# Optimization experiments

Measured on AMD Instinct MI355X. Metric: run time of the kernel, lower is better.

## Reference

```python
import jax, jax.numpy as jnp
import numpy as np

B, T, D, H = 2048, 512, 1, 36


def _lstm_dir(x, Wih, Whh, bih, bhh, reverse):
    # x: [B,T,Din]; Wih: [4H,Din]; Whh: [4H,H]. PyTorch gate order: i,f,g,o.
    # Precompute input projection for all timesteps (hoisted out of the scan).
    xp = jnp.einsum('btd,gd->btg', x, Wih) + (bih + bhh)  # [B,T,4H]
    xp = jnp.swapaxes(xp, 0, 1)  # [T,B,4H]
    if reverse:
        xp = xp[::-1]
    h0 = jnp.zeros((x.shape[0], Whh.shape[1]), x.dtype)

    def step(carry, xt):
        h, c = carry
        z = xt + h @ Whh.T  # [B,4H]
        i, f, g, o = jnp.split(z, 4, axis=-1)
        c = jax.nn.sigmoid(f) * c + jax.nn.sigmoid(i) * jnp.tanh(g)
        h = jax.nn.sigmoid(o) * jnp.tanh(c)
        return (h, c), h

    _, hs = jax.lax.scan(step, (h0, h0), xp)  # hs: [T,B,H]
    if reverse:
        hs = hs[::-1]
    return jnp.swapaxes(hs, 0, 1)  # [B,T,H]


def _bilstm_layer(x, pf, pr):
    hf = _lstm_dir(x, *pf, reverse=False)
    hr = _lstm_dir(x, *pr, reverse=True)
    return jnp.concatenate([hf, hr], axis=-1)  # [B,T,2H]


def setup_inputs() -> dict:
    key = jax.random.key(0)
    ks = jax.random.split(key, 20)
    bound = 1.0 / np.sqrt(H)  # PyTorch LSTM/Linear uniform init bound

    def u(k, shape):
        return jax.random.uniform(k, shape, jnp.float32, -bound, bound)

    inp = {"x": jax.random.normal(ks[0], (B, T, D), jnp.float32)}
    # layer 0 (input size D), forward and reverse directions
    inp["Wih0f"] = u(ks[1], (4 * H, D)); inp["Whh0f"] = u(ks[2], (4 * H, H))
    inp["bih0f"] = u(ks[3], (4 * H,));  inp["bhh0f"] = u(ks[4], (4 * H,))
    inp["Wih0r"] = u(ks[5], (4 * H, D)); inp["Whh0r"] = u(ks[6], (4 * H, H))
    inp["bih0r"] = u(ks[7], (4 * H,));  inp["bhh0r"] = u(ks[8], (4 * H,))
    # layer 1 (input size 2H)
    inp["Wih1f"] = u(ks[9], (4 * H, 2 * H)); inp["Whh1f"] = u(ks[10], (4 * H, H))
    inp["bih1f"] = u(ks[11], (4 * H,));      inp["bhh1f"] = u(ks[12], (4 * H,))
    inp["Wih1r"] = u(ks[13], (4 * H, 2 * H)); inp["Whh1r"] = u(ks[14], (4 * H, H))
    inp["bih1r"] = u(ks[15], (4 * H,));       inp["bhh1r"] = u(ks[16], (4 * H,))
    # fc head: Linear(2H -> 1)
    inp["fcW"] = u(ks[17], (1, 2 * H))
    inp["fcb"] = u(ks[18], (1,))
    return inp


def reference(x, Wih0f, Whh0f, bih0f, bhh0f, Wih0r, Whh0r, bih0r, bhh0r,
              Wih1f, Whh1f, bih1f, bhh1f, Wih1r, Whh1r, bih1r, bhh1r,
              fcW, fcb):
    out = _bilstm_layer(x, (Wih0f, Whh0f, bih0f, bhh0f),
                        (Wih0r, Whh0r, bih0r, bhh0r))
    out = _bilstm_layer(out, (Wih1f, Whh1f, bih1f, bhh1f),
                        (Wih1r, Whh1r, bih1r, bhh1r))
    return out[:, -1, :] @ fcW.T + fcb  # [B,1]
```

## Files before the change

kernel.cpp:

```cpp
#include <hip/hip_runtime.h>
#include <cstdint>

#define Hn 36
#define G4 144
#define TT 512
#define BB 2048

__device__ __forceinline__ float sigf(float x) { return 1.0f / (1.0f + __expf(-x)); }
__device__ __forceinline__ float tanh_fast(float x) {
    float e = __expf(2.0f * x);
    return 1.0f - 2.0f / (e + 1.0f);
}

#define REP9(M, P)  M(P,0) M(P,1) M(P,2) M(P,3) M(P,4) M(P,5) M(P,6) M(P,7) M(P,8)
#define DECLQ(P, i) float P##i##x, P##i##y, P##i##z, P##i##w;
#define LOADQ(P, i) { float4 _t = wp[i]; P##i##x = _t.x; P##i##y = _t.y; P##i##z = _t.z; P##i##w = _t.w; }
#define PINQ(P, i)  asm volatile("" : "+v"(P##i##x), "+v"(P##i##y), "+v"(P##i##z), "+v"(P##i##w));
#define FMAQ(P, i)                                                        \
    {  float4 hv = *(const float4*)&hb[(i) * 4];                          \
       z0 = fmaf(P##i##x, hv.x, z0); z1 = fmaf(P##i##y, hv.y, z1);        \
       z2 = fmaf(P##i##z, hv.z, z2); z3 = fmaf(P##i##w, hv.w, z3); }

#define DOT4Q(P, i)                                                       \
    {   float4 hA = *(const float4*)&hbb[0 * 40 + (i) * 4];               \
        A0 = fmaf(P##i##x, hA.x, A0); A1 = fmaf(P##i##y, hA.y, A1);       \
        A2 = fmaf(P##i##z, hA.z, A2); A3 = fmaf(P##i##w, hA.w, A3);       \
        float4 hB = *(const float4*)&hbb[1 * 40 + (i) * 4];               \
        B0 = fmaf(P##i##x, hB.x, B0); B1 = fmaf(P##i##y, hB.y, B1);       \
        B2 = fmaf(P##i##z, hB.z, B2); B3 = fmaf(P##i##w, hB.w, B3);       \
        float4 hC = *(const float4*)&hbb[2 * 40 + (i) * 4];               \
        C0 = fmaf(P##i##x, hC.x, C0); C1 = fmaf(P##i##y, hC.y, C1);       \
        C2 = fmaf(P##i##z, hC.z, C2); C3 = fmaf(P##i##w, hC.w, C3);       \
        float4 hD = *(const float4*)&hbb[3 * 40 + (i) * 4];               \
        D0 = fmaf(P##i##x, hD.x, D0); D1 = fmaf(P##i##y, hD.y, D1);       \
        D2 = fmaf(P##i##z, hD.z, D2); D3 = fmaf(P##i##w, hD.w, D3); }

#define DOT36(W, H, Z0, Z1, Z2, Z3)                        \
    do {                                                   \
        _Pragma("unroll") for (int _k = 0; _k < 9; ++_k) { \
            float4 hv = *(const float4*)&(H)[_k * 4];      \
            Z0 = fmaf((W)[_k * 4 + 0], hv.x, Z0);          \
            Z1 = fmaf((W)[_k * 4 + 1], hv.y, Z1);          \
            Z2 = fmaf((W)[_k * 4 + 2], hv.z, Z2);          \
            Z3 = fmaf((W)[_k * 4 + 3], hv.w, Z3);          \
        }                                                  \
    } while (0)

#define DOT72(W, H, Z0, Z1, Z2, Z3)                         \
    do {                                                    \
        _Pragma("unroll") for (int _k = 0; _k < 18; ++_k) { \
            float4 hv = *(const float4*)&(H)[_k * 4];       \
            Z0 = fmaf((W)[_k * 4 + 0], hv.x, Z0);           \
            Z1 = fmaf((W)[_k * 4 + 1], hv.y, Z1);           \
            Z2 = fmaf((W)[_k * 4 + 2], hv.z, Z2);           \
            Z3 = fmaf((W)[_k * 4 + 3], hv.w, Z3);           \
        }                                                   \
    } while (0)

#define SG1 4
#define NTK1 (SG1 * G4)
__global__ __launch_bounds__(NTK1) void l0rev_kernel(
    const float* __restrict__ x,
    const float* __restrict__ Wih, const float* __restrict__ Whh,
    const float* __restrict__ bih, const float* __restrict__ bhh,
    float* __restrict__ h0r)
{
    const int tid = threadIdx.x;
    const int cc  = tid / G4;
    const int g   = tid % G4;
    const int b   = blockIdx.x * SG1 + cc;

    __shared__ float xs[SG1][TT];
    __shared__ float hs[SG1][40];
    __shared__ float zs[SG1][G4];

    for (int i = g; i < TT; i += G4) xs[cc][i] = x[(size_t)b * TT + i];

    REP9(DECLQ, R)
    {
        const float4* wp = (const float4*)(Whh + g * Hn);
        REP9(LOADQ, R)
    }
    float wx   = Wih[g];
    float bias = bih[g] + bhh[g];
    REP9(PINQ, R)
    asm volatile("" : "+v"(wx), "+v"(bias));

    if (g < 40) hs[cc][g] = 0.0f;
    float c = 0.0f;
    __syncthreads();

    float* dst = h0r + (size_t)b * TT * Hn;

    for (int s = 0; s < TT; ++s) {
        const int t = TT - 1 - s;
        float z0 = fmaf(xs[cc][t], wx, bias), z1 = 0.f, z2 = 0.f, z3 = 0.f;
        {
            const float* hb = hs[cc];
            REP9(FMAQ, R)
        }
        zs[cc][g] = (z0 + z1) + (z2 + z3);
        __syncthreads();
        if (g < Hn) {
            float zi = zs[cc][g], zf = zs[cc][g + 36], zg = zs[cc][g + 72], zo = zs[cc][g + 108];
            c = sigf(zf) * c + sigf(zi) * tanh_fast(zg);
            float h = sigf(zo) * tanh_fast(c);
            hs[cc][g] = h;
            dst[(size_t)t * Hn + g] = h;
        }
        __syncthreads();
    }
}

#define SG2 4
#define NT2 576
__global__ __launch_bounds__(NT2) void fused_fl_kernel(
    const float* __restrict__ x,
    const float* __restrict__ Wih0f, const float* __restrict__ Whh0f,
    const float* __restrict__ bih0f, const float* __restrict__ bhh0f,
    const float* __restrict__ Wih1f, const float* __restrict__ Whh1f,
    const float* __restrict__ bih1f, const float* __restrict__ bhh1f,
    const float* __restrict__ Wih1r,
    const float* __restrict__ bih1r, const float* __restrict__ bhh1r,
    const float* __restrict__ fcW, const float* __restrict__ fcb,
    const float* __restrict__ h0r,
    float* __restrict__ out)
{
    const int tid  = threadIdx.x;
    const int gp   = tid / G4;
    const int g    = tid % G4;
    const int cc2  = g / Hn;
    const int ii   = g % Hn;
    const int base = blockIdx.x * SG2;

    __shared__ float xs[SG2][TT + 2];
    __shared__ float h0f[2][SG2][40];
    __shared__ float h0rs[2][SG2][40];
    __shared__ float h1s[SG2][40];
    __shared__ float zF[SG2][G4];
    __shared__ float zL[3][SG2][G4];
    __shared__ float red[SG2][40];

    for (int i = tid; i < SG2 * (TT + 2); i += NT2) {
        int c = i / (TT + 2), t = i % (TT + 2);
        xs[c][t] = (t < TT) ? x[(size_t)(base + c) * TT + t] : 0.0f;
    }
    for (int i = tid; i < 2 * SG2 * 40; i += NT2) {
        (&h0f[0][0][0])[i] = 0.0f;
        (&h0rs[0][0][0])[i] = 0.0f;
    }
    for (int i = tid; i < SG2 * 40; i += NT2) (&h1s[0][0])[i] = 0.0f;

    const float* wbase = (gp == 0) ? (Whh0f + g * Hn)
                       : (gp == 1) ? (Wih1f + g * 72)
                       : (gp == 2) ? (Wih1f + g * 72 + 36)
                                   : (Whh1f + g * Hn);
    REP9(DECLQ, W)
    {
        const float4* wp = (const float4*)wbase;
        REP9(LOADQ, W)
    }
    float wx0  = (gp == 0) ? Wih0f[g] : 0.0f;
    float bsum = (gp == 0) ? (bih0f[g] + bhh0f[g])
               : (gp == 3) ? (bih1f[g] + bhh1f[g]) : 0.0f;
    REP9(PINQ, W)
    asm volatile("" : "+v"(wx0), "+v"(bsum));

    const float* srow = h0r + (size_t)(base + cc2) * TT * Hn + ii;
    float c0 = 0.0f, c1 = 0.0f;
    __syncthreads();

    float rv = 0.0f;
    if (gp == 0) {
#pragma unroll
        for (int c = 0; c < SG2; ++c) zF[c][g] = fmaf(xs[c][0], wx0, bsum);
    } else if (gp == 2) {
        h0rs[0][cc2][ii] = srow[0];
        rv = srow[Hn];
    }
    __syncthreads();
    if (gp == 0) {
        float zi = zF[cc2][ii], zg = zF[cc2][ii + 72], zo = zF[cc2][ii + 108];
        c0 = sigf(zi) * tanh_fast(zg);
        h0f[0][cc2][ii] = sigf(zo) * tanh_fast(c0);
    }
    __syncthreads();

    int cur = 0;
    for (int t = 0; t < TT; ++t) {
        float rv2 = (gp == 2 && t + 2 < TT) ? srow[(size_t)(t + 2) * Hn] : 0.0f;

        const float* hbb = (gp <= 1) ? &h0f[cur][0][0]
                         : (gp == 2) ? &h0rs[cur][0][0] : &h1s[0][0];
        float A0, B0, C0, D0;
        if (gp == 0) {
            A0 = fmaf(xs[0][t + 1], wx0, bsum);
            B0 = fmaf(xs[1][t + 1], wx0, bsum);
            C0 = fmaf(xs[2][t + 1], wx0, bsum);
            D0 = fmaf(xs[3][t + 1], wx0, bsum);
        } else {
            A0 = bsum; B0 = bsum; C0 = bsum; D0 = bsum;
        }
        float A1 = 0.f, A2 = 0.f, A3 = 0.f, B1 = 0.f, B2 = 0.f, B3 = 0.f;
        float C1 = 0.f, C2 = 0.f, C3 = 0.f, D1 = 0.f, D2 = 0.f, D3 = 0.f;

        REP9(DOT4Q, W)

        float zA = (A0 + A1) + (A2 + A3);
        float zB = (B0 + B1) + (B2 + B3);
        float zC = (C0 + C1) + (C2 + C3);
        float zD = (D0 + D1) + (D2 + D3);
        if (gp == 0) {
            zF[0][g] = zA; zF[1][g] = zB; zF[2][g] = zC; zF[3][g] = zD;
        } else {
            float* zt = &zL[gp - 1][0][0];
            zt[0 * G4 + g] = zA; zt[1 * G4 + g] = zB;
            zt[2 * G4 + g] = zC; zt[3 * G4 + g] = zD;
        }
        __syncthreads();

        if (gp == 0) {
            if (t + 1 < TT) {
                float zi = zF[cc2][ii],       zf = zF[cc2][ii + 36];
                float zg = zF[cc2][ii + 72],  zo = zF[cc2][ii + 108];
                c0 = sigf(zf) * c0 + sigf(zi) * tanh_fast(zg);
                h0f[cur ^ 1][cc2][ii] = sigf(zo) * tanh_fast(c0);
            }
        } else if (gp == 3) {
            float zi = zL[0][cc2][ii]       + zL[1][cc2][ii]       + zL[2][cc2][ii];
            float zf = zL[0][cc2][ii + 36]  + zL[1][cc2][ii + 36]  + zL[2][cc2][ii + 36];
            float zg = zL[0][cc2][ii + 72]  + zL[1][cc2][ii + 72]  + zL[2][cc2][ii + 72];
            float zo = zL[0][cc2][ii + 108] + zL[1][cc2][ii + 108] + zL[2][cc2][ii + 108];
            c1 = sigf(zf) * c1 + sigf(zi) * tanh_fast(zg);
            h1s[cc2][ii] = sigf(zo) * tanh_fast(c1);
        } else if (gp == 2 && t + 1 < TT) {
            h0rs[cur ^ 1][cc2][ii] = rv;
        }
        __syncthreads();
        rv = rv2;
        if (t + 1 < TT) cur ^= 1;
    }

    {
        float zR = bih1r[g] + bhh1r[g];
        const float* wr = Wih1r + g * 72;
#pragma unroll
        for (int k = 0; k < Hn; ++k) zR = fmaf(wr[k],      h0f[cur][gp][k],  zR);
#pragma unroll
        for (int k = 0; k < Hn; ++k) zR = fmaf(wr[36 + k], h0rs[cur][gp][k], zR);
        zF[gp][g] = zR;
    }
    __syncthreads();
    if (tid < SG2 * Hn) {
        int c = tid / Hn, i = tid % Hn;
        float zi = zF[c][i], zg = zF[c][i + 72], zo = zF[c][i + 108];
        float cR = sigf(zi) * tanh_fast(zg);
        float hR = sigf(zo) * tanh_fast(cR);
        red[c][i] = fcW[36 + i] * hR + fcW[i] * h1s[c][i];
    }
    __syncthreads();
    if (tid < SG2) {
        float s2 = fcb[0];
        for (int j = 0; j < Hn; ++j) s2 += red[tid][j];
        out[base + tid] = s2;
    }
}

__global__ __launch_bounds__(G4, 1) void fused_all_kernel(
    const float* __restrict__ x,
    const float* __restrict__ Wih0f, const float* __restrict__ Whh0f,
    const float* __restrict__ bih0f, const float* __restrict__ bhh0f,
    const float* __restrict__ Wih0r, const float* __restrict__ Whh0r,
    const float* __restrict__ bih0r, const float* __restrict__ bhh0r,
    const float* __restrict__ Wih1f, const float* __restrict__ Whh1f,
    const float* __restrict__ bih1f, const float* __restrict__ bhh1f,
    const float* __restrict__ Wih1r,
    const float* __restrict__ bih1r, const float* __restrict__ bhh1r,
    const float* __restrict__ fcW, const float* __restrict__ fcb,
    float* __restrict__ out)
{
    const int g = threadIdx.x;
    const int b = blockIdx.x;

    __shared__ float xs[TT];
    __shared__ float cbuf[64][Hn];
    __shared__ float ckpt_h[8][Hn], ckpt_c[8][Hn];
    __shared__ float hr[40], h0s[80], hs1[40], zs[G4], red[40];

    for (int i = g; i < TT; i += G4) xs[i] = x[(size_t)b * TT + i];

    float wr[Hn], wf[Hn];
#pragma unroll
    for (int k = 0; k < Hn; ++k) wr[k] = Whh0r[g * Hn + k];
#pragma unroll
    for (int k = 0; k < Hn; ++k) wf[k] = Whh0f[g * Hn + k];
    const float wxr = Wih0r[g], br = bih0r[g] + bhh0r[g];
    const float wxf = Wih0f[g], bf = bih0f[g] + bhh0f[g];
    float w1i[72];
#pragma unroll
    for (int k = 0; k < 72; ++k) w1i[k] = Wih1f[g * 72 + k];
    float w1h[Hn];
#pragma unroll
    for (int k = 0; k < Hn; ++k) w1h[k] = Whh1f[g * Hn + k];
    const float b1 = bih1f[g] + bhh1f[g];

    if (g < Hn) hr[g] = 0.0f;
    float cr = 0.0f;
    __syncthreads();
    for (int s = 0; s < TT; ++s) {
        const int t = TT - 1 - s;
        if ((t & 63) == 63 && g < Hn) { ckpt_h[t >> 6][g] = hr[g]; ckpt_c[t >> 6][g] = cr; }
        float z0 = fmaf(xs[t], wxr, br), z1 = 0.f, z2 = 0.f, z3 = 0.f;
        DOT36(wr, hr, z0, z1, z2, z3);
        zs[g] = (z0 + z1) + (z2 + z3);
        __syncthreads();
        if (g < Hn) {
            float zi = zs[g], zf = zs[g + 36], zg = zs[g + 72], zo = zs[g + 108];
            cr = sigf(zf) * cr + sigf(zi) * tanh_fast(zg);
            hr[g] = sigf(zo) * tanh_fast(cr);
        }
        __syncthreads();
    }

    if (g < Hn) { h0s[g] = 0.0f; hs1[g] = 0.0f; }
    float c0 = 0.0f, c1 = 0.0f;
    __syncthreads();

    for (int m = 0; m < 8; ++m) {
        if (g < Hn) { hr[g] = ckpt_h[m][g]; cr = ckpt_c[m][g]; }
        __syncthreads();
        for (int j = 0; j < 64; ++j) {
            const int t = m * 64 + 63 - j;
            float z0 = fmaf(xs[t], wxr, br), z1 = 0.f, z2 = 0.f, z3 = 0.f;
            DOT36(wr, hr, z0, z1, z2, z3);
            zs[g] = (z0 + z1) + (z2 + z3);
            __syncthreads();
            if (g < Hn) {
                float zi = zs[g], zf = zs[g + 36], zg = zs[g + 72], zo = zs[g + 108];
                cr = sigf(zf) * cr + sigf(zi) * tanh_fast(zg);
                float h = sigf(zo) * tanh_fast(cr);
                hr[g] = h;
                cbuf[t & 63][g] = h;
            }
            __syncthreads();
        }
        for (int j = 0; j < 64; ++j) {
            const int t = m * 64 + j;
            float z0 = fmaf(xs[t], wxf, bf), z1 = 0.f, z2 = 0.f, z3 = 0.f;
            DOT36(wf, h0s, z0, z1, z2, z3);
            zs[g] = (z0 + z1) + (z2 + z3);
            __syncthreads();
            if (g < Hn) {
                float zi = zs[g], zf = zs[g + 36], zg = zs[g + 72], zo = zs[g + 108];
                c0 = sigf(zf) * c0 + sigf(zi) * tanh_fast(zg);
                h0s[g] = sigf(zo) * tanh_fast(c0);
            } else if (g < 72) {
                h0s[g] = cbuf[j][g - 36];
            }
            __syncthreads();
            float y0 = b1, y1 = 0.f, y2 = 0.f, y3 = 0.f;
            DOT72(w1i, h0s, y0, y1, y2, y3);
            DOT36(w1h, hs1, y0, y1, y2, y3);
            zs[g] = (y0 + y1) + (y2 + y3);
            __syncthreads();
            if (g < Hn) {
                float zi = zs[g], zf = zs[g + 36], zg = zs[g + 72], zo = zs[g + 108];
                c1 = sigf(zf) * c1 + sigf(zi) * tanh_fast(zg);
                hs1[g] = sigf(zo) * tanh_fast(c1);
            }
            __syncthreads();
        }
    }

    float zR = bih1r[g] + bhh1r[g];
#pragma unroll
    for (int k = 0; k < 72; ++k) zR = fmaf(Wih1r[g * 72 + k], h0s[k], zR);
    zs[g] = zR;
    __syncthreads();
    if (g < Hn) {
        float zi = zs[g], zg = zs[g + 72], zo = zs[g + 108];
        float c  = sigf(zi) * tanh_fast(zg);
        float hrv = sigf(zo) * tanh_fast(c);
        red[g] = fcW[36 + g] * hrv + fcW[g] * hs1[g];
    }
    __syncthreads();
    if (g == 0) {
        float s = fcb[0];
        for (int j = 0; j < Hn; ++j) s += red[j];
        out[b] = s;
    }
}

extern "C" void kernel_launch(void* const* d_in, const int* in_sizes, int n_in,
                              void* d_out, int out_size, void* d_ws, size_t ws_size,
                              hipStream_t stream)
{
    const float* x     = (const float*)d_in[0];
    const float* Wih0f = (const float*)d_in[1];
    const float* Whh0f = (const float*)d_in[2];
    const float* bih0f = (const float*)d_in[3];
    const float* bhh0f = (const float*)d_in[4];
    const float* Wih0r = (const float*)d_in[5];
    const float* Whh0r = (const float*)d_in[6];
    const float* bih0r = (const float*)d_in[7];
    const float* bhh0r = (const float*)d_in[8];
    const float* Wih1f = (const float*)d_in[9];
    const float* Whh1f = (const float*)d_in[10];
    const float* bih1f = (const float*)d_in[11];
    const float* bhh1f = (const float*)d_in[12];
    const float* Wih1r = (const float*)d_in[13];
    const float* bih1r = (const float*)d_in[15];
    const float* bhh1r = (const float*)d_in[16];
    const float* fcW   = (const float*)d_in[17];
    const float* fcb   = (const float*)d_in[18];

    const size_t need = (size_t)BB * TT * Hn * sizeof(float);
    if (d_ws != nullptr && ws_size >= need) {
        float* h0r = (float*)d_ws;
        l0rev_kernel<<<BB / SG1, NTK1, 0, stream>>>(x, Wih0r, Whh0r, bih0r, bhh0r, h0r);
        fused_fl_kernel<<<BB / SG2, NT2, 0, stream>>>(
            x, Wih0f, Whh0f, bih0f, bhh0f, Wih1f, Whh1f, bih1f, bhh1f,
            Wih1r, bih1r, bhh1r, fcW, fcb, h0r, (float*)d_out);
    } else {
        fused_all_kernel<<<BB, G4, 0, stream>>>(
            x, Wih0f, Whh0f, bih0f, bhh0f, Wih0r, Whh0r, bih0r, bhh0r,
            Wih1f, Whh1f, bih1f, bhh1f, Wih1r, bih1r, bhh1r, fcW, fcb,
            (float*)d_out);
    }
}
```

Before: 2.036 ms.

## Restructure fused layer kernel: per-hidden-unit threads, smem weights, shuffle reduce, 8 sequences

Remaps threads of the fused forward-layer0/layer1 kernel so each thread owns one hidden unit's four gates for one sequence, with the K dimension split in halves across lane pairs and combined via a lane shuffle. Weights move from registers into transposed float4 shared-memory arrays, and the z-exchange through shared memory plus the first barrier of every timestep is removed, leaving one barrier per step. The block now processes 8 sequences instead of 4, halving the grid. The trade is more shared-memory weight traffic per step and higher LDS use per block, which may lower occupancy.

```diff
diff --git a/kernel.cpp b/kernel.cpp
--- a/kernel.cpp
+++ b/kernel.cpp
@@ -20,20 +20,6 @@
     {  float4 hv = *(const float4*)&hb[(i) * 4];                          \
        z0 = fmaf(P##i##x, hv.x, z0); z1 = fmaf(P##i##y, hv.y, z1);        \
        z2 = fmaf(P##i##z, hv.z, z2); z3 = fmaf(P##i##w, hv.w, z3); }
-
-#define DOT4Q(P, i)                                                       \
-    {   float4 hA = *(const float4*)&hbb[0 * 40 + (i) * 4];               \
-        A0 = fmaf(P##i##x, hA.x, A0); A1 = fmaf(P##i##y, hA.y, A1);       \
-        A2 = fmaf(P##i##z, hA.z, A2); A3 = fmaf(P##i##w, hA.w, A3);       \
-        float4 hB = *(const float4*)&hbb[1 * 40 + (i) * 4];               \
-        B0 = fmaf(P##i##x, hB.x, B0); B1 = fmaf(P##i##y, hB.y, B1);       \
-        B2 = fmaf(P##i##z, hB.z, B2); B3 = fmaf(P##i##w, hB.w, B3);       \
-        float4 hC = *(const float4*)&hbb[2 * 40 + (i) * 4];               \
-        C0 = fmaf(P##i##x, hC.x, C0); C1 = fmaf(P##i##y, hC.y, C1);       \
-        C2 = fmaf(P##i##z, hC.z, C2); C3 = fmaf(P##i##w, hC.w, C3);       \
-        float4 hD = *(const float4*)&hbb[3 * 40 + (i) * 4];               \
-        D0 = fmaf(P##i##x, hD.x, D0); D1 = fmaf(P##i##y, hD.y, D1);       \
-        D2 = fmaf(P##i##z, hD.z, D2); D3 = fmaf(P##i##w, hD.w, D3); }
 
 #define DOT36(W, H, Z0, Z1, Z2, Z3)                        \
     do {                                                   \
@@ -112,8 +98,11 @@
     }
 }
 
-#define SG2 4
+#define SG2 8
 #define NT2 576
+#define NB2 (BB / SG2)
+#define HST 44
+
 __global__ __launch_bounds__(NT2) void fused_fl_kernel(
     const float* __restrict__ x,
     const float* __restrict__ Wih0f, const float* __restrict__ Whh0f,
@@ -127,136 +116,175 @@
     float* __restrict__ out)
 {
     const int tid  = threadIdx.x;
-    const int gp   = tid / G4;
-    const int g    = tid % G4;
-    const int cc2  = g / Hn;
-    const int ii   = g % Hn;
+    const int u    = tid >> 4;
+    const int part = (tid >> 3) & 1;
+    const int ch   = tid & 7;
     const int base = blockIdx.x * SG2;
 
+    __shared__ float4 wt0t[10 * G4];
+    __shared__ float4 wt1t[18 * G4];
+    __shared__ float4 wt3t[10 * G4];
     __shared__ float xs[SG2][TT + 2];
-    __shared__ float h0f[2][SG2][40];
-    __shared__ float h0rs[2][SG2][40];
-    __shared__ float h1s[SG2][40];
-    __shared__ float zF[SG2][G4];
-    __shared__ float zL[3][SG2][G4];
-    __shared__ float red[SG2][40];
-
+    __shared__ float h0fb[2][SG2][HST];
+    __shared__ float h0rb[2][SG2][HST];
+    __shared__ float h1b[2][SG2][HST];
+    __shared__ float ztail[SG2][G4];
+    __shared__ float red[SG2][Hn];
+
+    for (int i = tid; i < 10 * G4; i += NT2) {
+        int q = i / G4, r = i % G4;
+        float4 z4; z4.x = 0.f; z4.y = 0.f; z4.z = 0.f; z4.w = 0.f;
+        wt0t[i] = (q < 9) ? ((const float4*)(Whh0f + r * Hn))[q] : z4;
+        wt3t[i] = (q < 9) ? ((const float4*)(Whh1f + r * Hn))[q] : z4;
+    }
+    for (int i = tid; i < 18 * G4; i += NT2) {
+        int q = i / G4, r = i % G4;
+        wt1t[i] = ((const float4*)(Wih1f + r * 72))[q];
+    }
     for (int i = tid; i < SG2 * (TT + 2); i += NT2) {
         int c = i / (TT + 2), t = i % (TT + 2);
         xs[c][t] = (t < TT) ? x[(size_t)(base + c) * TT + t] : 0.0f;
     }
-    for (int i = tid; i < 2 * SG2 * 40; i += NT2) {
-        (&h0f[0][0][0])[i] = 0.0f;
-        (&h0rs[0][0][0])[i] = 0.0f;
-    }
-    for (int i = tid; i < SG2 * 40; i += NT2) (&h1s[0][0])[i] = 0.0f;
-
-    const float* wbase = (gp == 0) ? (Whh0f + g * Hn)
-                       : (gp == 1) ? (Wih1f + g * 72)
-                       : (gp == 2) ? (Wih1f + g * 72 + 36)
-                                   : (Whh1f + g * Hn);
-    REP9(DECLQ, W)
-    {
-        const float4* wp = (const float4*)wbase;
-        REP9(LOADQ, W)
-    }
-    float wx0  = (gp == 0) ? Wih0f[g] : 0.0f;
-    float bsum = (gp == 0) ? (bih0f[g] + bhh0f[g])
-               : (gp == 3) ? (bih1f[g] + bhh1f[g]) : 0.0f;
-    REP9(PINQ, W)
-    asm volatile("" : "+v"(wx0), "+v"(bsum));
-
-    const float* srow = h0r + (size_t)(base + cc2) * TT * Hn + ii;
-    float c0 = 0.0f, c1 = 0.0f;
-    __syncthreads();
-
-    float rv = 0.0f;
-    if (gp == 0) {
-#pragma unroll
-        for (int c = 0; c < SG2; ++c) zF[c][g] = fmaf(xs[c][0], wx0, bsum);
-    } else if (gp == 2) {
-        h0rs[0][cc2][ii] = srow[0];
-        rv = srow[Hn];
-    }
-    __syncthreads();
-    if (gp == 0) {
-        float zi = zF[cc2][ii], zg = zF[cc2][ii + 72], zo = zF[cc2][ii + 108];
+    for (int i = tid; i < 2 * SG2 * HST; i += NT2) {
+        (&h0fb[0][0][0])[i] = 0.0f;
+        (&h0rb[0][0][0])[i] = 0.0f;
+        (&h1b[0][0][0])[i]  = 0.0f;
+    }
+
+    const int r0 = u, r1 = u + 36, r2 = u + 72, r3 = u + 108;
+    float wxi = 0.f, wxf = 0.f, wxg = 0.f, wxo = 0.f;
+    float bi, bf_, bg_, bo;
+    if (part == 0) {
+        wxi = Wih0f[r0]; wxf = Wih0f[r1]; wxg = Wih0f[r2]; wxo = Wih0f[r3];
+        bi  = bih0f[r0] + bhh0f[r0]; bf_ = bih0f[r1] + bhh0f[r1];
+        bg_ = bih0f[r2] + bhh0f[r2]; bo  = bih0f[r3] + bhh0f[r3];
+    } else {
+        bi  = bih1f[r0] + bhh1f[r0]; bf_ = bih1f[r1] + bhh1f[r1];
+        bg_ = bih1f[r2] + bhh1f[r2]; bo  = bih1f[r3] + bhh1f[r3];
+    }
+
+    const float4* w0b = wt0t + (part * 5) * G4;
+    const float4* w1b = wt1t + (part * 9) * G4;
+    const float4* w3b = wt3t + (part * 5) * G4;
+    const int hq0 = part * 5 * 4;
+
+    const float* srow = h0r + (size_t)(base + ch) * TT * Hn + u;
+    float c0 = 0.f, c1 = 0.f, rvv = 0.f;
+    __syncthreads();
+
+    if (part == 0) {
+        float x0 = xs[ch][0];
+        float zi = fmaf(x0, wxi, bi), zg = fmaf(x0, wxg, bg_), zo = fmaf(x0, wxo, bo);
         c0 = sigf(zi) * tanh_fast(zg);
-        h0f[0][cc2][ii] = sigf(zo) * tanh_fast(c0);
+        h0fb[0][ch][u] = sigf(zo) * tanh_fast(c0);
+    } else {
+        h0rb[0][ch][u] = srow[0];
+        rvv = srow[Hn];
     }
     __syncthreads();
 
     int cur = 0;
     for (int t = 0; t < TT; ++t) {
-        float rv2 = (gp == 2 && t + 2 < TT) ? srow[(size_t)(t + 2) * Hn] : 0.0f;
-
-        const float* hbb = (gp <= 1) ? &h0f[cur][0][0]
-                         : (gp == 2) ? &h0rs[cur][0][0] : &h1s[0][0];
-        float A0, B0, C0, D0;
-        if (gp == 0) {
-            A0 = fmaf(xs[0][t + 1], wx0, bsum);
-            B0 = fmaf(xs[1][t + 1], wx0, bsum);
-            C0 = fmaf(xs[2][t + 1], wx0, bsum);
-            D0 = fmaf(xs[3][t + 1], wx0, bsum);
+        float rv2 = (part == 1 && t + 2 < TT) ? srow[(size_t)(t + 2) * Hn] : 0.0f;
+
+        const float* h0c = &h0fb[cur][ch][0];
+        const float* hrc = &h0rb[cur][ch][0];
+        const float* h1c = &h1b[cur][ch][0];
+        const float* hsrc = part ? hrc : h0c;
+
+        float zA = 0.f, zB = 0.f, zC = 0.f, zD = 0.f;
+        float yA = 0.f, yB = 0.f, yC = 0.f, yD = 0.f;
+
+#pragma unroll
+        for (int i = 0; i < 5; ++i) {
+            float4 w_0 = w0b[i * G4 + r0], w_1 = w0b[i * G4 + r1];
+            float4 w_2 = w0b[i * G4 + r2], w_3 = w0b[i * G4 + r3];
+            float4 h = *(const float4*)&h0c[hq0 + i * 4];
+            zA = fmaf(w_0.x, h.x, zA); zA = fmaf(w_0.y, h.y, zA);
+            zA = fmaf(w_0.z, h.z, zA); zA = fmaf(w_0.w, h.w, zA);
+            zB = fmaf(w_1.x, h.x, zB); zB = fmaf(w_1.y, h.y, zB);
+            zB = fmaf(w_1.z, h.z, zB); zB = fmaf(w_1.w, h.w, zB);
+            zC = fmaf(w_2.x, h.x, zC); zC = fmaf(w_2.y, h.y, zC);
+            zC = fmaf(w_2.z, h.z, zC); zC = fmaf(w_2.w, h.w, zC);
+            zD = fmaf(w_3.x, h.x, zD); zD = fmaf(w_3.y, h.y, zD);
+            zD = fmaf(w_3.z, h.z, zD); zD = fmaf(w_3.w, h.w, zD);
+        }
+#pragma unroll
+        for (int i = 0; i < 9; ++i) {
+            float4 w_0 = w1b[i * G4 + r0], w_1 = w1b[i * G4 + r1];
+            float4 w_2 = w1b[i * G4 + r2], w_3 = w1b[i * G4 + r3];
+            float4 h = *(const float4*)&hsrc[i * 4];
+            yA = fmaf(w_0.x, h.x, yA); yA = fmaf(w_0.y, h.y, yA);
+            yA = fmaf(w_0.z, h.z, yA); yA = fmaf(w_0.w, h.w, yA);
+            yB = fmaf(w_1.x, h.x, yB); yB = fmaf(w_1.y, h.y, yB);
+            yB = fmaf(w_1.z, h.z, yB); yB = fmaf(w_1.w, h.w, yB);
+            yC = fmaf(w_2.x, h.x, yC); yC = fmaf(w_2.y, h.y, yC);
+            yC = fmaf(w_2.z, h.z, yC); yC = fmaf(w_2.w, h.w, yC);
+            yD = fmaf(w_3.x, h.x, yD); yD = fmaf(w_3.y, h.y, yD);
+            yD = fmaf(w_3.z, h.z, yD); yD = fmaf(w_3.w, h.w, yD);
+        }
+#pragma unroll
+        for (int i = 0; i < 5; ++i) {
+            float4 w_0 = w3b[i * G4 + r0], w_1 = w3b[i * G4 + r1];
+            float4 w_2 = w3b[i * G4 + r2], w_3 = w3b[i * G4 + r3];
+            float4 h = *(const float4*)&h1c[hq0 + i * 4];
+            yA = fmaf(w_0.x, h.x, yA); yA = fmaf(w_0.y, h.y, yA);
+            yA = fmaf(w_0.z, h.z, yA); yA = fmaf(w_0.w, h.w, yA);
+            yB = fmaf(w_1.x, h.x, yB); yB = fmaf(w_1.y, h.y, yB);
+            yB = fmaf(w_1.z, h.z, yB); yB = fmaf(w_1.w, h.w, yB);
+            yC = fmaf(w_2.x, h.x, yC); yC = fmaf(w_2.y, h.y, yC);
+            yC = fmaf(w_2.z, h.z, yC); yC = fmaf(w_2.w, h.w, yC);
+            yD = fmaf(w_3.x, h.x, yD); yD = fmaf(w_3.y, h.y, yD);
+            yD = fmaf(w_3.z, h.z, yD); yD = fmaf(w_3.w, h.w, yD);
+        }
+
+        zA += __shfl_xor(zA, 8); zB += __shfl_xor(zB, 8);
+        zC += __shfl_xor(zC, 8); zD += __shfl_xor(zD, 8);
+        yA += __shfl_xor(yA, 8); yB += __shfl_xor(yB, 8);
+        yC += __shfl_xor(yC, 8); yD += __shfl_xor(yD, 8);
+
+        if (part == 0) {
+            if (t + 1 < TT) {
+                float xn = xs[ch][t + 1];
+                float zi = fmaf(xn, wxi, bi)  + zA;
+                float zf = fmaf(xn, wxf, bf_) + zB;
+                float zg = fmaf(xn, wxg, bg_) + zC;
+                float zo = fmaf(xn, wxo, bo)  + zD;
+                c0 = sigf(zf) * c0 + sigf(zi) * tanh_fast(zg);
+                h0fb[cur ^ 1][ch][u] = sigf(zo) * tanh_fast(c0);
+            }
         } else {
-            A0 = bsum; B0 = bsum; C0 = bsum; D0 = bsum;
-        }
-        float A1 = 0.f, A2 = 0.f, A3 = 0.f, B1 = 0.f, B2 = 0.f, B3 = 0.f;
-        float C1 = 0.f, C2 = 0.f, C3 = 0.f, D1 = 0.f, D2 = 0.f, D3 = 0.f;
-
-        REP9(DOT4Q, W)
-
-        float zA = (A0 + A1) + (A2 + A3);
-        float zB = (B0 + B1) + (B2 + B3);
-        float zC = (C0 + C1) + (C2 + C3);
-        float zD = (D0 + D1) + (D2 + D3);
-        if (gp == 0) {
-            zF[0][g] = zA; zF[1][g] = zB; zF[2][g] = zC; zF[3][g] = zD;
-        } else {
-            float* zt = &zL[gp - 1][0][0];
-            zt[0 * G4 + g] = zA; zt[1 * G4 + g] = zB;
-            zt[2 * G4 + g] = zC; zt[3 * G4 + g] = zD;
-        }
-        __syncthreads();
-
-        if (gp == 0) {
-            if (t + 1 < TT) {
-                float zi = zF[cc2][ii],       zf = zF[cc2][ii + 36];
-                float zg = zF[cc2][ii + 72],  zo = zF[cc2][ii + 108];
-                c0 = sigf(zf) * c0 + sigf(zi) * tanh_fast(zg);
-                h0f[cur ^ 1][cc2][ii] = sigf(zo) * tanh_fast(c0);
-            }
-        } else if (gp == 3) {
-            float zi = zL[0][cc2][ii]       + zL[1][cc2][ii]       + zL[2][cc2][ii];
-            float zf = zL[0][cc2][ii + 36]  + zL[1][cc2][ii + 36]  + zL[2][cc2][ii + 36];
-            float zg = zL[0][cc2][ii + 72]  + zL[1][cc2][ii + 72]  + zL[2][cc2][ii + 72];
-            float zo = zL[0][cc2][ii + 108] + zL[1][cc2][ii + 108] + zL[2][cc2][ii + 108];
+            float zi = yA + bi, zf = yB + bf_, zg = yC + bg_, zo = yD + bo;
             c1 = sigf(zf) * c1 + sigf(zi) * tanh_fast(zg);
-            h1s[cc2][ii] = sigf(zo) * tanh_fast(c1);
-        } else if (gp == 2 && t + 1 < TT) {
-            h0rs[cur ^ 1][cc2][ii] = rv;
-        }
-        __syncthreads();
-        rv = rv2;
-        if (t + 1 < TT) cur ^= 1;
+            h1b[cur ^ 1][ch][u] = sigf(zo) * tanh_fast(c1);
+            if (t + 1 < TT) h0rb[cur ^ 1][ch][u] = rvv;
+            rvv = rv2;
+        }
+        __syncthreads();
+        cur ^= 1;
     }
 
     {
-        float zR = bih1r[g] + bhh1r[g];
-        const float* wr = Wih1r + g * 72;
-#pragma unroll
-        for (int k = 0; k < Hn; ++k) zR = fmaf(wr[k],      h0f[cur][gp][k],  zR);
-#pragma unroll
-        for (int k = 0; k < Hn; ++k) zR = fmaf(wr[36 + k], h0rs[cur][gp][k], zR);
-        zF[gp][g] = zR;
-    }
-    __syncthreads();
-    if (tid < SG2 * Hn) {
-        int c = tid / Hn, i = tid % Hn;
-        float zi = zF[c][i], zg = zF[c][i + 72], zo = zF[c][i + 108];
+        const int gpT = tid / G4, gT = tid % G4;
+#pragma unroll
+        for (int s2 = 0; s2 < 2; ++s2) {
+            const int cc = gpT * 2 + s2;
+            float zR = bih1r[gT] + bhh1r[gT];
+            const float* wrq = Wih1r + gT * 72;
+#pragma unroll
+            for (int k = 0; k < Hn; ++k) zR = fmaf(wrq[k],      h0fb[1][cc][k], zR);
+#pragma unroll
+            for (int k = 0; k < Hn; ++k) zR = fmaf(wrq[36 + k], h0rb[1][cc][k], zR);
+            ztail[cc][gT] = zR;
+        }
+    }
+    __syncthreads();
+    if (tid < 288) {
+        const int c2 = tid / 36, i2 = tid % 36;
+        float zi = ztail[c2][i2], zg = ztail[c2][i2 + 72], zo = ztail[c2][i2 + 108];
         float cR = sigf(zi) * tanh_fast(zg);
         float hR = sigf(zo) * tanh_fast(cR);
-        red[c][i] = fcW[36 + i] * hR + fcW[i] * h1s[c][i];
+        red[c2][i2] = fcW[36 + i2] * hR + fcW[i2] * h1b[0][c2][i2];
     }
     __syncthreads();
     if (tid < SG2) {
@@ -418,7 +446,7 @@
     if (d_ws != nullptr && ws_size >= need) {
         float* h0r = (float*)d_ws;
         l0rev_kernel<<<BB / SG1, NTK1, 0, stream>>>(x, Wih0r, Whh0r, bih0r, bhh0r, h0r);
-        fused_fl_kernel<<<BB / SG2, NT2, 0, stream>>>(
+        fused_fl_kernel<<<NB2, NT2, 0, stream>>>(
             x, Wih0f, Whh0f, bih0f, bhh0f, Wih1f, Whh1f, bih1f, bhh1f,
             Wih1r, bih1r, bhh1r, fcW, fcb, h0r, (float*)d_out);
     } else {
```

Measured after the change: 2.720 ms. 33.6% more time.
